# Kernel tuning notes

Measured on AMD Instinct MI355X. Metric: run time of the kernel, lower is better.

Reference implementation:

```python
import jax, jax.numpy as jnp
import numpy as np

N_NODES = 20000
N_EDGES = 320000
IN_FEATS = 256
H_FEATS = 256


def setup_inputs() -> dict:
    key = jax.random.key(0)
    ks = jax.random.split(key, 8)
    s = 1.0 / np.sqrt(IN_FEATS)
    return {
        "features": jax.random.normal(ks[0], (N_NODES, IN_FEATS), jnp.float32),
        "src": jax.random.randint(ks[1], (N_EDGES,), 0, N_NODES, jnp.int32),
        "dst": jax.random.randint(ks[2], (N_EDGES,), 0, N_NODES, jnp.int32),
        "W_self1": jax.random.normal(ks[3], (IN_FEATS, H_FEATS), jnp.float32) * s,
        "W_neigh1": jax.random.normal(ks[4], (IN_FEATS, H_FEATS), jnp.float32) * s,
        "b1": jnp.zeros((H_FEATS,), jnp.float32),
        "W_self2": jax.random.normal(ks[5], (H_FEATS, H_FEATS), jnp.float32) * s,
        "W_neigh2": jax.random.normal(ks[6], (H_FEATS, H_FEATS), jnp.float32) * s,
        "b2": jnp.zeros((H_FEATS,), jnp.float32),
    }


def _sage_conv(h, src, dst, W_self, W_neigh, b, n_nodes):
    # mean aggregation of src features onto dst nodes (DGL SAGEConv 'mean')
    msg_sum = jax.ops.segment_sum(h[src], dst, num_segments=n_nodes)  # [N, d]
    deg = jax.ops.segment_sum(jnp.ones_like(dst, dtype=h.dtype), dst,
                              num_segments=n_nodes)  # [N]
    h_neigh = msg_sum / jnp.maximum(deg, 1.0)[:, None]  # isolated nodes -> 0
    return h @ W_self + h_neigh @ W_neigh + b


def reference(features, src, dst, W_self1, W_neigh1, b1, W_self2, W_neigh2, b2):
    n = features.shape[0]
    h = _sage_conv(features, src, dst, W_self1, W_neigh1, b1, n)
    h = jax.nn.relu(h)
    h = _sage_conv(h, src, dst, W_self2, W_neigh2, b2, n)
    # DotPredictor: per-edge dot product of src/dst embeddings
    score = jnp.sum(h[src] * h[dst], axis=1)  # [E]
    return score
```

## Files before the change

kernel.cpp:

```cpp
#include <hip/hip_runtime.h>
#include <hip/hip_bf16.h>
#include <stdint.h>

typedef __bf16 bf16_t;
typedef __bf16 bf16x8 __attribute__((ext_vector_type(8)));
typedef __bf16 bf16x4 __attribute__((ext_vector_type(4)));
typedef float f32x4 __attribute__((ext_vector_type(4)));

#define NFEAT 256
#define KDIM  512
#define BM 64
#define BN 128
#define BK 64

__device__ __forceinline__ void gload_lds16(const void* g, void* l) {
  __builtin_amdgcn_global_load_lds(
      (const __attribute__((address_space(1))) unsigned int*)g,
      (__attribute__((address_space(3))) unsigned int*)l, 16, 0, 0);
}


__global__ void k_count_deg(const int* __restrict__ dst, int* __restrict__ deg, int nE) {
  int i = blockIdx.x * blockDim.x + threadIdx.x;
  if (i < nE) atomicAdd(&deg[dst[i]], 1);
}


__global__ __launch_bounds__(256) void k_scan_part(const int* __restrict__ deg,
                                                   int* __restrict__ partial, int n) {
  const int tid = threadIdx.x;
  int i = blockIdx.x * 256 + tid;
  int d = (i < n) ? deg[i] : 0;
  #pragma unroll
  for (int off = 32; off; off >>= 1) d += __shfl_xor(d, off, 64);
  __shared__ int ws[4];
  if ((tid & 63) == 0) ws[tid >> 6] = d;
  __syncthreads();
  if (tid == 0) partial[blockIdx.x] = ws[0] + ws[1] + ws[2] + ws[3];
}

__global__ __launch_bounds__(256) void k_scan_mid(int* __restrict__ partial, int nb) {
  __shared__ int s[256];
  const int tid = threadIdx.x;
  int d = (tid < nb) ? partial[tid] : 0;
  s[tid] = d;
  __syncthreads();
  for (int off = 1; off < 256; off <<= 1) {
    int v = (tid >= off) ? s[tid - off] : 0;
    __syncthreads();
    s[tid] += v;
    __syncthreads();
  }
  if (tid < nb) partial[tid] = s[tid] - d;
}

__global__ __launch_bounds__(256) void k_scan_final(const int* __restrict__ deg,
                                                    const int* __restrict__ partial,
                                                    int* __restrict__ offsets,
                                                    int* __restrict__ cursor,
                                                    float* __restrict__ inv_deg, int n) {
  __shared__ int s[256];
  const int tid = threadIdx.x;
  int i = blockIdx.x * 256 + tid;
  int d = (i < n) ? deg[i] : 0;
  s[tid] = d;
  __syncthreads();
  for (int off = 1; off < 256; off <<= 1) {
    int v = (tid >= off) ? s[tid - off] : 0;
    __syncthreads();
    s[tid] += v;
    __syncthreads();
  }
  if (i < n) {
    int excl = partial[blockIdx.x] + s[tid] - d;
    offsets[i] = excl;
    cursor[i]  = excl;
    inv_deg[i] = 1.0f / (float)(d > 1 ? d : 1);
  }
}

__global__ void k_scatter(const int* __restrict__ src, const int* __restrict__ dst,
                          int* __restrict__ cursor, int* __restrict__ csr_src, int nE) {
  int i = blockIdx.x * blockDim.x + threadIdx.x;
  if (i < nE) {
    int pos = atomicAdd(&cursor[dst[i]], 1);
    csr_src[pos] = src[i];
  }
}

__global__ void k_prep(const float* __restrict__ F,
                       const float* __restrict__ Ws1, const float* __restrict__ Wn1,
                       const float* __restrict__ Ws2, const float* __restrict__ Wn2,
                       bf16_t* __restrict__ WT1, bf16_t* __restrict__ WT2,
                       bf16_t* __restrict__ X,
                       int* __restrict__ deg, int nNodes, int mpad) {
  int t = blockIdx.x * blockDim.x + threadIdx.x;
  if (t < mpad) deg[t] = 0;
  if (t < 2 * NFEAT * KDIM) {
    int layer = t >> 17;
    int r = t & (NFEAT * KDIM - 1);
    int n = r >> 9;
    int k = r & 511;
    const float* Ws = layer ? Ws2 : Ws1;
    const float* Wn = layer ? Wn2 : Wn1;
    float v = (k < NFEAT) ? Ws[k * NFEAT + n] : Wn[(k - NFEAT) * NFEAT + n];
    (layer ? WT2 : WT1)[r] = (bf16_t)v;
  }
  int n = t >> 6;
  int c = (t & 63) * 4;
  if (n < mpad) {
    float4 v = make_float4(0.f, 0.f, 0.f, 0.f);
    if (n < nNodes) v = *(const float4*)&F[(size_t)n * NFEAT + c];
    bf16x4 o;
    o[0] = (bf16_t)v.x; o[1] = (bf16_t)v.y; o[2] = (bf16_t)v.z; o[3] = (bf16_t)v.w;
    *(bf16x4*)&X[(size_t)n * KDIM + c] = o;
  }
}

__global__ __launch_bounds__(256) void k_agg(const bf16_t* __restrict__ Hin,
                                             bf16_t* __restrict__ Hout,
                                             const int* __restrict__ csr_src,
                                             const int* __restrict__ offsets,
                                             const int* __restrict__ deg,
                                             const float* __restrict__ inv_deg,
                                             int instride, int outstride) {
  const int n = blockIdx.x * 4 + (threadIdx.x >> 6);
  const int lane = threadIdx.x & 63;
  const int half = lane >> 5;
  const int l32 = lane & 31;
  const int beg = offsets[n];
  const int cnt = deg[n];
  const size_t colo = (size_t)l32 * 8;

  float acc[8] = {0.f, 0.f, 0.f, 0.f, 0.f, 0.f, 0.f, 0.f};

  int s_cur = (half < cnt) ? csr_src[beg + half] : -1;
  for (int i = 0; i < cnt; i += 2) {
    int k1 = i + 2 + half;
    int s_nxt = (k1 < cnt) ? csr_src[beg + k1] : -1;
    if (s_cur >= 0) {
      bf16x8 v = *(const bf16x8*)&Hin[(size_t)s_cur * instride + colo];
      #pragma unroll
      for (int j = 0; j < 8; ++j) acc[j] += (float)v[j];
    }
    s_cur = s_nxt;
  }

  #pragma unroll
  for (int j = 0; j < 8; ++j) acc[j] += __shfl_xor(acc[j], 32, 64);

  if (half == 0) {
    float w = inv_deg[n];
    bf16x8 o;
    #pragma unroll
    for (int j = 0; j < 8; ++j) o[j] = (bf16_t)(acc[j] * w);
    *(bf16x8*)&Hout[(size_t)n * outstride + NFEAT + colo] = o;
  }
}

__global__ __launch_bounds__(256, 3) void k_gemm(const bf16_t* __restrict__ A,
                                                 const bf16_t* __restrict__ BT,
                                                 const float* __restrict__ bias,
                                                 bf16_t* __restrict__ Cout,
                                                 int ostride, int relu) {
  __shared__ __align__(16) bf16_t As[2][BM * BK];
  __shared__ __align__(16) bf16_t Bs[2][BN * BK];
  const int tid  = threadIdx.x;
  const int lane = tid & 63;
  const int wave = tid >> 6;
  const int wr = wave >> 1, wc = wave & 1;
  const int m0 = blockIdx.x * BM;
  const int n0 = blockIdx.y * BN;
  const int l15 = lane & 15;
  const int lk8 = (lane >> 4) * 8;

  f32x4 acc[2][4] = {};

  auto stage = [&](int buf, int kt) {
    const int k0 = kt * BK;
    #pragma unroll
    for (int i = 0; i < 2; ++i) {
      int idx = i * 256 + tid;
      int row = idx >> 3;
      int c8  = (idx & 7) * 8;
      gload_lds16(A + (size_t)(m0 + row) * KDIM + k0 + c8,
                  (char*)&As[buf][0] + (i * 256 + wave * 64) * 16);
    }
    #pragma unroll
    for (int i = 0; i < 4; ++i) {
      int idx = i * 256 + tid;
      int row = idx >> 3;
      int c8  = (idx & 7) * 8;
      gload_lds16(BT + (size_t)(n0 + row) * KDIM + k0 + c8,
                  (char*)&Bs[buf][0] + (i * 256 + wave * 64) * 16);
    }
  };

  auto compute = [&](int buf) {
    #pragma unroll
    for (int kk = 0; kk < 2; ++kk) {
      bf16x8 af[2], bfr[4];
      #pragma unroll
      for (int m = 0; m < 2; ++m) {
        int row = wr * 32 + m * 16 + l15;
        af[m] = *(const bf16x8*)&As[buf][row * BK + kk * 32 + lk8];
      }
      #pragma unroll
      for (int n = 0; n < 4; ++n) {
        int col = wc * 64 + n * 16 + l15;
        bfr[n] = *(const bf16x8*)&Bs[buf][col * BK + kk * 32 + lk8];
      }
      #pragma unroll
      for (int m = 0; m < 2; ++m)
        #pragma unroll
        for (int n = 0; n < 4; ++n)
          acc[m][n] = __builtin_amdgcn_mfma_f32_16x16x32_bf16(af[m], bfr[n], acc[m][n], 0, 0, 0);
    }
  };

  stage(0, 0);
  __syncthreads();
  const int nt = KDIM / BK;
  int cur = 0;
  for (int t = 0; t < nt; ++t) {
    if (t + 1 < nt) stage(cur ^ 1, t + 1);
    compute(cur);
    __syncthreads();
    cur ^= 1;
  }

  #pragma unroll
  for (int n = 0; n < 4; ++n) {
    int col = n0 + wc * 64 + n * 16 + l15;
    float bv = bias[col];
    #pragma unroll
    for (int m = 0; m < 2; ++m) {
      int rbase = m0 + wr * 32 + m * 16 + (lane >> 4) * 4;
      #pragma unroll
      for (int j = 0; j < 4; ++j) {
        float v = acc[m][n][j] + bv;
        if (relu) v = fmaxf(v, 0.f);
        Cout[(size_t)(rbase + j) * ostride + col] = (bf16_t)v;
      }
    }
  }
}

__global__ __launch_bounds__(256) void k_edge_dot(const bf16_t* __restrict__ H,
                                                  const int* __restrict__ src,
                                                  const int* __restrict__ dst,
                                                  float* __restrict__ out, int nE) {
  const int wid  = (blockIdx.x * blockDim.x + threadIdx.x) >> 6;
  const int lane = threadIdx.x & 63;
  const int l15  = lane & 15;
  const int hi   = lane >> 4;
  const int e0   = wid * 16;
  if (e0 >= nE) return;
  int es = e0 + l15;
  if (es >= nE) es = nE - 1;

  const int s = src[es], d = dst[es];
  const bf16_t* ps = H + (size_t)s * NFEAT + hi * 8;
  const bf16_t* pd = H + (size_t)d * NFEAT + hi * 8;

  f32x4 acc = {0.f, 0.f, 0.f, 0.f};
  #pragma unroll
  for (int ks = 0; ks < 8; ++ks) {
    bf16x8 a = *(const bf16x8*)(ps + ks * 32);
    bf16x8 b = *(const bf16x8*)(pd + ks * 32);
    acc = __builtin_amdgcn_mfma_f32_16x16x32_bf16(a, b, acc, 0, 0, 0);
  }

  if ((l15 >> 2) == hi && (e0 + l15) < nE) {
    int j = l15 & 3;
    float v = acc[0];
    v = (j == 1) ? acc[1] : v;
    v = (j == 2) ? acc[2] : v;
    v = (j == 3) ? acc[3] : v;
    out[e0 + l15] = v;
  }
}


extern "C" void kernel_launch(void* const* d_in, const int* in_sizes, int n_in,
                              void* d_out, int out_size, void* d_ws, size_t ws_size,
                              hipStream_t stream) {
  const float* features = (const float*)d_in[0];
  const int*   src      = (const int*)d_in[1];
  const int*   dst      = (const int*)d_in[2];
  const float* Wself1   = (const float*)d_in[3];
  const float* Wneigh1  = (const float*)d_in[4];
  const float* b1       = (const float*)d_in[5];
  const float* Wself2   = (const float*)d_in[6];
  const float* Wneigh2  = (const float*)d_in[7];
  const float* b2       = (const float*)d_in[8];
  float* score = (float*)d_out;

  const int nNodes = in_sizes[0] / NFEAT;
  const int nE     = in_sizes[1];
  const int mpad   = ((nNodes + 127) / 128) * 128;

  char* ws = (char*)d_ws;
  size_t off = 0;
  auto alloc = [&](size_t bytes) { char* p = ws + off; off += (bytes + 255) & ~(size_t)255; return p; };
  bf16_t* Xcat1   = (bf16_t*)alloc((size_t)mpad * KDIM * 2);
  bf16_t* Xcat2   = (bf16_t*)alloc((size_t)mpad * KDIM * 2);
  bf16_t* H2      = (bf16_t*)alloc((size_t)mpad * NFEAT * 2);
  bf16_t* WT1     = (bf16_t*)alloc((size_t)NFEAT * KDIM * 2);
  bf16_t* WT2     = (bf16_t*)alloc((size_t)NFEAT * KDIM * 2);
  int*    deg     = (int*)alloc((size_t)mpad * 4);
  int*    offsets = (int*)alloc((size_t)mpad * 4);
  int*    cursor  = (int*)alloc((size_t)mpad * 4);
  float*  inv_deg = (float*)alloc((size_t)mpad * 4);
  int*    csr_src = (int*)alloc((size_t)nE * 4);
  int*    partial = (int*)alloc(1024 * 4);

  const int eb = (nE + 255) / 256;
  const int nb = (mpad + 255) / 256;

  k_prep<<<(mpad * 64 + 255) / 256, 256, 0, stream>>>(features, Wself1, Wneigh1,
                                                      Wself2, Wneigh2, WT1, WT2,
                                                      Xcat1, deg, nNodes, mpad);

  k_count_deg<<<eb, 256, 0, stream>>>(dst, deg, nE);
  k_scan_part<<<nb, 256, 0, stream>>>(deg, partial, mpad);
  k_scan_mid<<<1, 256, 0, stream>>>(partial, nb);
  k_scan_final<<<nb, 256, 0, stream>>>(deg, partial, offsets, cursor, inv_deg, mpad);
  k_scatter<<<eb, 256, 0, stream>>>(src, dst, cursor, csr_src, nE);

  k_agg<<<mpad / 4, 256, 0, stream>>>(Xcat1, Xcat1, csr_src, offsets, deg, inv_deg, KDIM, KDIM);
  dim3 ggrid(mpad / BM, NFEAT / BN);
  k_gemm<<<ggrid, 256, 0, stream>>>(Xcat1, WT1, b1, Xcat2, KDIM, 1);

  k_agg<<<mpad / 4, 256, 0, stream>>>(Xcat2, Xcat2, csr_src, offsets, deg, inv_deg, KDIM, KDIM);
  k_gemm<<<ggrid, 256, 0, stream>>>(Xcat2, WT2, b2, H2, NFEAT, 0);

  const int nWaves = (nE + 15) / 16;
  k_edge_dot<<<(nWaves + 3) / 4, 256, 0, stream>>>(H2, src, dst, score, nE);
}
```

Baseline: 166.5 us.

## Process edge dot in dst-sorted order and use half-wave per node aggregation

The scatter pass now also writes a packed (src, dst, edge id) record in CSR order. The edge-dot kernel walks edges in destination-sorted order so the dst rows are reused and cached, and it writes results back through the original edge index. The aggregation kernel now gives each node a 32-lane half wave that loads two neighbor rows per iteration, where before a full wave split neighbors between its halves and combined them with a shuffle. The cost is an extra 16-byte-per-edge write in the scatter and scattered output stores in edge-dot.

```diff
diff --git a/kernel.cpp b/kernel.cpp
--- a/kernel.cpp
+++ b/kernel.cpp
@@ -80,11 +80,15 @@
 }
 
 __global__ void k_scatter(const int* __restrict__ src, const int* __restrict__ dst,
-                          int* __restrict__ cursor, int* __restrict__ csr_src, int nE) {
+                          int* __restrict__ cursor, int* __restrict__ csr_src,
+                          int4* __restrict__ csr_pack, int nE) {
   int i = blockIdx.x * blockDim.x + threadIdx.x;
   if (i < nE) {
-    int pos = atomicAdd(&cursor[dst[i]], 1);
-    csr_src[pos] = src[i];
+    int d = dst[i];
+    int s = src[i];
+    int pos = atomicAdd(&cursor[d], 1);
+    csr_src[pos]  = s;
+    csr_pack[pos] = make_int4(s, d, i, 0);
   }
 }
 
@@ -124,38 +128,39 @@
                                              const int* __restrict__ deg,
                                              const float* __restrict__ inv_deg,
                                              int instride, int outstride) {
-  const int n = blockIdx.x * 4 + (threadIdx.x >> 6);
-  const int lane = threadIdx.x & 63;
-  const int half = lane >> 5;
-  const int l32 = lane & 31;
+  const int n   = blockIdx.x * 8 + (threadIdx.x >> 5);
+  const int l32 = threadIdx.x & 31;
   const int beg = offsets[n];
   const int cnt = deg[n];
   const size_t colo = (size_t)l32 * 8;
 
   float acc[8] = {0.f, 0.f, 0.f, 0.f, 0.f, 0.f, 0.f, 0.f};
 
-  int s_cur = (half < cnt) ? csr_src[beg + half] : -1;
+  int s0 = (0 < cnt) ? csr_src[beg] : -1;
+  int s1 = (1 < cnt) ? csr_src[beg + 1] : -1;
   for (int i = 0; i < cnt; i += 2) {
-    int k1 = i + 2 + half;
-    int s_nxt = (k1 < cnt) ? csr_src[beg + k1] : -1;
-    if (s_cur >= 0) {
-      bf16x8 v = *(const bf16x8*)&Hin[(size_t)s_cur * instride + colo];
-      #pragma unroll
-      for (int j = 0; j < 8; ++j) acc[j] += (float)v[j];
-    }
-    s_cur = s_nxt;
-  }
-
+    bf16x8 v0, v1;
+    const bool h0 = (s0 >= 0), h1 = (s1 >= 0);
+    if (h0) v0 = *(const bf16x8*)&Hin[(size_t)s0 * instride + colo];
+    if (h1) v1 = *(const bf16x8*)&Hin[(size_t)s1 * instride + colo];
+    int j = i + 2;
+    s0 = (j < cnt)     ? csr_src[beg + j]     : -1;
+    s1 = (j + 1 < cnt) ? csr_src[beg + j + 1] : -1;
+    if (h0) {
+      #pragma unroll
+      for (int q = 0; q < 8; ++q) acc[q] += (float)v0[q];
+    }
+    if (h1) {
+      #pragma unroll
+      for (int q = 0; q < 8; ++q) acc[q] += (float)v1[q];
+    }
+  }
+
+  float w = inv_deg[n];
+  bf16x8 o;
   #pragma unroll
-  for (int j = 0; j < 8; ++j) acc[j] += __shfl_xor(acc[j], 32, 64);
-
-  if (half == 0) {
-    float w = inv_deg[n];
-    bf16x8 o;
-    #pragma unroll
-    for (int j = 0; j < 8; ++j) o[j] = (bf16_t)(acc[j] * w);
-    *(bf16x8*)&Hout[(size_t)n * outstride + NFEAT + colo] = o;
-  }
+  for (int q = 0; q < 8; ++q) o[q] = (bf16_t)(acc[q] * w);
+  *(bf16x8*)&Hout[(size_t)n * outstride + NFEAT + colo] = o;
 }
 
 __global__ __launch_bounds__(256, 3) void k_gemm(const bf16_t* __restrict__ A,
@@ -247,8 +252,7 @@
 }
 
 __global__ __launch_bounds__(256) void k_edge_dot(const bf16_t* __restrict__ H,
-                                                  const int* __restrict__ src,
-                                                  const int* __restrict__ dst,
+                                                  const int4* __restrict__ csr_pack,
                                                   float* __restrict__ out, int nE) {
   const int wid  = (blockIdx.x * blockDim.x + threadIdx.x) >> 6;
   const int lane = threadIdx.x & 63;
@@ -256,12 +260,12 @@
   const int hi   = lane >> 4;
   const int e0   = wid * 16;
   if (e0 >= nE) return;
-  int es = e0 + l15;
-  if (es >= nE) es = nE - 1;
-
-  const int s = src[es], d = dst[es];
-  const bf16_t* ps = H + (size_t)s * NFEAT + hi * 8;
-  const bf16_t* pd = H + (size_t)d * NFEAT + hi * 8;
+  int pos = e0 + l15;
+  if (pos >= nE) pos = nE - 1;
+
+  const int4 e = csr_pack[pos];
+  const bf16_t* ps = H + (size_t)e.x * NFEAT + hi * 8;
+  const bf16_t* pd = H + (size_t)e.y * NFEAT + hi * 8;
 
   f32x4 acc = {0.f, 0.f, 0.f, 0.f};
   #pragma unroll
@@ -277,7 +281,7 @@
     v = (j == 1) ? acc[1] : v;
     v = (j == 2) ? acc[2] : v;
     v = (j == 3) ? acc[3] : v;
-    out[e0 + l15] = v;
+    out[e.z] = v;
   }
 }
 
@@ -313,6 +317,7 @@
   int*    cursor  = (int*)alloc((size_t)mpad * 4);
   float*  inv_deg = (float*)alloc((size_t)mpad * 4);
   int*    csr_src = (int*)alloc((size_t)nE * 4);
+  int4*   csr_pack= (int4*)alloc((size_t)nE * 16);
   int*    partial = (int*)alloc(1024 * 4);
 
   const int eb = (nE + 255) / 256;
@@ -326,15 +331,15 @@
   k_scan_part<<<nb, 256, 0, stream>>>(deg, partial, mpad);
   k_scan_mid<<<1, 256, 0, stream>>>(partial, nb);
   k_scan_final<<<nb, 256, 0, stream>>>(deg, partial, offsets, cursor, inv_deg, mpad);
-  k_scatter<<<eb, 256, 0, stream>>>(src, dst, cursor, csr_src, nE);
-
-  k_agg<<<mpad / 4, 256, 0, stream>>>(Xcat1, Xcat1, csr_src, offsets, deg, inv_deg, KDIM, KDIM);
+  k_scatter<<<eb, 256, 0, stream>>>(src, dst, cursor, csr_src, csr_pack, nE);
+
+  k_agg<<<mpad / 8, 256, 0, stream>>>(Xcat1, Xcat1, csr_src, offsets, deg, inv_deg, KDIM, KDIM);
   dim3 ggrid(mpad / BM, NFEAT / BN);
   k_gemm<<<ggrid, 256, 0, stream>>>(Xcat1, WT1, b1, Xcat2, KDIM, 1);
 
-  k_agg<<<mpad / 4, 256, 0, stream>>>(Xcat2, Xcat2, csr_src, offsets, deg, inv_deg, KDIM, KDIM);
+  k_agg<<<mpad / 8, 256, 0, stream>>>(Xcat2, Xcat2, csr_src, offsets, deg, inv_deg, KDIM, KDIM);
   k_gemm<<<ggrid, 256, 0, stream>>>(Xcat2, WT2, b2, H2, NFEAT, 0);
 
   const int nWaves = (nE + 15) / 16;
-  k_edge_dot<<<(nWaves + 3) / 4, 256, 0, stream>>>(H2, src, dst, score, nE);
-}
+  k_edge_dot<<<(nWaves + 3) / 4, 256, 0, stream>>>(H2, csr_pack, score, nE);
+}
```

New measurement: 157.0 us. 5.7% less time.
